# Kernel optimization log

Measured on AMD Instinct MI355X. Metric: run time of the kernel, lower is better.

Reference implementation:

```python
import jax, jax.numpy as jnp
import numpy as np

N = 50000   # nodes
E = 1000000 # edges
D = 64      # input_nf = output_nf = hidden_nf
COORDS_WEIGHT = 1.0


def setup_inputs() -> dict:
    key = jax.random.key(0)
    ks = jax.random.split(key, 16)
    h = jax.random.normal(ks[0], (N, D), dtype=jnp.float32)
    coord = jax.random.normal(ks[1], (N, 3), dtype=jnp.float32)
    edge_index = jax.random.randint(ks[2], (2, E), 0, N, dtype=jnp.int32)
    s = 0.05  # generic init scale
    # edge_mlp: Linear(2D+1 -> D), ReLU, Linear(D -> D), ReLU
    We1 = jax.random.normal(ks[3], (2 * D + 1, D), dtype=jnp.float32) * s
    be1 = jnp.zeros((D,), dtype=jnp.float32)
    We2 = jax.random.normal(ks[4], (D, D), dtype=jnp.float32) * s
    be2 = jnp.zeros((D,), dtype=jnp.float32)
    # node_mlp: Linear(2D -> D), ReLU, Linear(D -> D)
    Wn1 = jax.random.normal(ks[5], (2 * D, D), dtype=jnp.float32) * s
    bn1 = jnp.zeros((D,), dtype=jnp.float32)
    Wn2 = jax.random.normal(ks[6], (D, D), dtype=jnp.float32) * s
    bn2 = jnp.zeros((D,), dtype=jnp.float32)
    # coord_mlp: Linear(D -> D), ReLU, Linear(D -> 1, no bias, xavier gain 0.001)
    Wc1 = jax.random.normal(ks[7], (D, D), dtype=jnp.float32) * s
    bc1 = jnp.zeros((D,), dtype=jnp.float32)
    Wc2 = jax.random.normal(ks[8], (D, 1), dtype=jnp.float32) * 0.001
    return {"h": h, "coord": coord, "edge_index": edge_index,
            "We1": We1, "be1": be1, "We2": We2, "be2": be2,
            "Wn1": Wn1, "bn1": bn1, "Wn2": Wn2, "bn2": bn2,
            "Wc1": Wc1, "bc1": bc1, "Wc2": Wc2}


def reference(h, coord, edge_index, We1, be1, We2, be2, Wn1, bn1, Wn2, bn2, Wc1, bc1, Wc2):
    row, col = edge_index[0], edge_index[1]
    # coord2radial (no PBC offsets; plain pairwise difference)
    coord_diff = coord[row] - coord[col]                    # [E, 3]
    radial = jnp.sum(coord_diff ** 2, axis=1, keepdims=True)  # [E, 1]

    # edge model: MLP on [h_i, h_j, ||x_i - x_j||^2]
    e_in = jnp.concatenate([h[row], h[col], radial], axis=1)  # [E, 2D+1]
    m = jax.nn.relu(e_in @ We1 + be1)
    edge_feat = jax.nn.relu(m @ We2 + be2)                   # [E, D]

    # coord model: per-edge scalar gate, clamp, segment mean
    gate = jax.nn.relu(edge_feat @ Wc1 + bc1) @ Wc2          # [E, 1]
    trans = jnp.clip(coord_diff * gate, -100.0, 100.0)       # [E, 3]
    trans_sum = jax.ops.segment_sum(trans, row, num_segments=N)  # [N, 3]
    cnt = jax.ops.segment_sum(jnp.ones((row.shape[0],), dtype=trans.dtype), row, num_segments=N)
    coord_out = (trans_sum / jnp.maximum(cnt, 1.0)[:, None]) * COORDS_WEIGHT  # [N, 3]

    # node model: scatter-sum aggregate then MLP with residual
    agg = jax.ops.segment_sum(edge_feat, row, num_segments=N)  # [N, D]
    n_in = jnp.concatenate([h, agg], axis=1)                   # [N, 2D]
    h_out = h + (jax.nn.relu(n_in @ Wn1 + bn1) @ Wn2 + bn2)    # residual
    return (h_out, coord_out)
```

## Files before the change

### kernel.cpp

```cpp
#include <hip/hip_runtime.h>

typedef float  f32x4  __attribute__((ext_vector_type(4)));
typedef __bf16 bf16x8 __attribute__((ext_vector_type(8)));
typedef unsigned short u16x8 __attribute__((ext_vector_type(8)));
typedef unsigned int   u32x4 __attribute__((ext_vector_type(4)));

__device__ inline unsigned short f2b(float f) {
    unsigned u = __builtin_bit_cast(unsigned, f);
    u += 0x7fffu + ((u >> 16) & 1u);
    return (unsigned short)(u >> 16);
}

__device__ inline unsigned cvtpk(float a, float b) {
    unsigned r;
    asm("v_cvt_pk_bf16_f32 %0, %1, %2" : "=v"(r) : "v"(a), "v"(b));
    return r;
}

__device__ inline f32x4 mfma16(bf16x8 a, bf16x8 b, f32x4 c) {
    return __builtin_amdgcn_mfma_f32_16x16x32_bf16(a, b, c, 0, 0, 0);
}

__device__ inline bf16x8 cvt8(f32x4 a, f32x4 b) {
    u32x4 w;
    w[0] = cvtpk(a[0], a[1]); w[1] = cvtpk(a[2], a[3]);
    w[2] = cvtpk(b[0], b[1]); w[3] = cvtpk(b[2], b[3]);
    return __builtin_bit_cast(bf16x8, w);
}

__device__ inline bf16x8 ldsA(const unsigned short* base, int frag, int lane) {
    return __builtin_bit_cast(bf16x8,
        *reinterpret_cast<const u16x8*>(base + ((frag * 64 + lane) << 3)));
}

__device__ inline void atom_pk(unsigned short* p, unsigned d) {
    asm volatile("global_atomic_pk_add_bf16 %0, %1, off" :: "v"(p), "v"(d) : "memory");
}

__global__ void k_prep(const float* __restrict__ h, unsigned short* __restrict__ hb,
                       u16x8* __restrict__ aggb8,
                       const int* __restrict__ erow, int* __restrict__ cnt,
                       int n8, int E)
{
    int i = blockIdx.x * 256 + threadIdx.x;
    if (i < n8) {
        const f32x4* p = reinterpret_cast<const f32x4*>(h + (size_t)i * 8);
        bf16x8 v = cvt8(p[0], p[1]);
        reinterpret_cast<u16x8*>(hb)[i] = __builtin_bit_cast(u16x8, v);
        aggb8[i] = (u16x8){0, 0, 0, 0, 0, 0, 0, 0};
    }
    if (i < E) atomicAdd(&cnt[erow[i]], 1);
}

__global__ void k_scanA(const int* __restrict__ cnt, int* __restrict__ bsum, int N)
{
    const int b = blockIdx.x, t = threadIdx.x;
    const int chunk = (N + gridDim.x - 1) / gridDim.x;
    const int lo = b * chunk;
    const int hi = min(lo + chunk, N);
    int s = 0;
    for (int i = lo + t; i < hi; i += 256) s += cnt[i];
#pragma unroll
    for (int d = 1; d < 64; d <<= 1) s += __shfl_xor(s, d, 64);
    __shared__ int ws[4];
    if ((t & 63) == 0) ws[t >> 6] = s;
    __syncthreads();
    if (t == 0) bsum[b] = ws[0] + ws[1] + ws[2] + ws[3];
}

__global__ void k_scanB(const int* __restrict__ cnt, const int* __restrict__ bsum,
                        int* __restrict__ woff, int N)
{
    const int b = blockIdx.x, t = threadIdx.x;
    __shared__ int base_sh;
    __shared__ int ws[4];
    {
        int v = (t < 128 && t < b) ? bsum[t] : 0;
#pragma unroll
        for (int d = 1; d < 64; d <<= 1) v += __shfl_xor(v, d, 64);
        if ((t & 63) == 0) ws[t >> 6] = v;
        __syncthreads();
        if (t == 0) base_sh = ws[0] + ws[1] + ws[2] + ws[3];
        __syncthreads();
    }
    const int base = base_sh;
    const int chunk = (N + gridDim.x - 1) / gridDim.x;
    const int lo = b * chunk;
    const int hi = min(lo + chunk, N);
    const int tchunk = (chunk + 255) / 256;
    const int tlo = lo + t * tchunk;
    const int thi = min(tlo + tchunk, hi);
    int s = 0;
    for (int i = tlo; i < thi; ++i) s += cnt[i];
    const int lane = t & 63, wv = t >> 6;
    int sc = s;
#pragma unroll
    for (int d = 1; d < 64; d <<= 1) { int u = __shfl_up(sc, d, 64); if (lane >= d) sc += u; }
    __shared__ int ws2[4];
    if (lane == 63) ws2[wv] = sc;
    __syncthreads();
    int wadd = 0;
#pragma unroll
    for (int k = 0; k < 4; ++k) wadd += (k < wv) ? ws2[k] : 0;
    int run = base + wadd + (sc - s);
    for (int i = tlo; i < thi; ++i) { woff[i] = run; run += cnt[i]; }
}

__global__ void k_scatter(const int* __restrict__ erow, const int* __restrict__ ecol,
                          int* __restrict__ woff, unsigned* __restrict__ spack,
                          float* __restrict__ cacc, int N, int E)
{
    int i = blockIdx.x * 256 + threadIdx.x;
    if (i < N)
        *reinterpret_cast<f32x4*>(cacc + (size_t)i * 4) = (f32x4){0.f, 0.f, 0.f, 0.f};
    if (i < E) {
        int r = erow[i];
        int pos = atomicAdd(&woff[r], 1);
        spack[pos] = (unsigned)r | ((unsigned)ecol[i] << 16);
    }
}

__global__ __launch_bounds__(512, 2) void egcl_edge_srt(
    const unsigned short* __restrict__ hb,
    const float* __restrict__ coord,
    const unsigned* __restrict__ spack,
    const float* __restrict__ We1, const float* __restrict__ be1,
    const float* __restrict__ We2, const float* __restrict__ be2,
    const float* __restrict__ Wc1, const float* __restrict__ bc1,
    const float* __restrict__ Wc2,
    unsigned short* __restrict__ aggb, float* __restrict__ cacc, int E)
{
    __shared__ __align__(16) unsigned short A1[16 * 512];
    __shared__ __align__(16) unsigned short A2[8 * 512];
    __shared__ __align__(16) unsigned short A3[8 * 512];
    __shared__ __align__(16) float bv[5][64];
    __shared__ __align__(16) unsigned stl[8][34 * 16];

    const int t = threadIdx.x;
    for (int i = t; i < 8192; i += 512) {
        int j = i & 7, lane = (i >> 3) & 63, fi = i >> 9;
        int mt = fi >> 2, ks = fi & 3;
        int in_ch = ks * 32 + ((lane >> 4) << 3) + j;
        int out   = mt * 16 + (lane & 15);
        A1[i] = f2b(We1[in_ch * 64 + out]);
    }
    for (int i = t; i < 4096; i += 512) {
        int j = i & 7, lane = (i >> 3) & 63, fi = i >> 9;
        int mt = fi >> 1, ks = fi & 1;
        int c   = (ks * 2 + (j >> 2)) * 16 + ((lane >> 4) & 3) * 4 + (j & 3);
        int out = mt * 16 + (lane & 15);
        A2[i] = f2b(We2[c * 64 + out]);
        A3[i] = f2b(Wc1[c * 64 + out]);
    }
    if (t < 64) {
        bv[0][t] = be1[t]; bv[1][t] = We1[128 * 64 + t];
        bv[2][t] = be2[t]; bv[3][t] = bc1[t]; bv[4][t] = Wc2[t];
    }
    __syncthreads();

    const int lane = t & 63;
    const int l16 = lane & 15, lq = lane >> 4;
    const int stride = gridDim.x * 8;
    const int wid = (blockIdx.x << 3) + (t >> 6);
    const int ntile = E >> 4;
    const int last = ntile - 1;
    unsigned* st = stl[t >> 6];

    int tile = wid;
    if (tile >= ntile) return;

    int eC = (tile << 4) + l16;
    unsigned pC = spack[eC];
    int rC = (int)(pC & 0xffffu), cC = (int)(pC >> 16);
    u16x8 hr0, hr1, hc0, hc1;
    {
        const u16x8* hr = reinterpret_cast<const u16x8*>(hb + (size_t)rC * 64);
        const u16x8* hc = reinterpret_cast<const u16x8*>(hb + (size_t)cC * 64);
        hr0 = hr[lq]; hr1 = hr[4 + lq]; hc0 = hc[lq]; hc1 = hc[4 + lq];
    }
    float px = 0.f, py = 0.f, pz = 0.f;
    if (lq < 2) {
        int node = (lq == 0) ? rC : cC;
        const float* pp = coord + (size_t)node * 3;
        px = pp[0]; py = pp[1]; pz = pp[2];
    }
    int t1 = tile + stride;
    int tn = (t1 < ntile) ? t1 : last;
    unsigned pN = spack[(tn << 4) + l16];
    int rN = (int)(pN & 0xffffu), cN = (int)(pN >> 16);

    for (; tile < ntile; ) {
        u16x8 nr0, nr1, nc0, nc1;
        {
            const u16x8* hr = reinterpret_cast<const u16x8*>(hb + (size_t)rN * 64);
            const u16x8* hc = reinterpret_cast<const u16x8*>(hb + (size_t)cN * 64);
            nr0 = hr[lq]; nr1 = hr[4 + lq]; nc0 = hc[lq]; nc1 = hc[4 + lq];
        }
        float npx = 0.f, npy = 0.f, npz = 0.f;
        if (lq < 2) {
            int node = (lq == 0) ? rN : cN;
            const float* pp = coord + (size_t)node * 3;
            npx = pp[0]; npy = pp[1]; npz = pp[2];
        }
        int t2 = tile + 2 * stride;
        int t2c = (t2 < ntile) ? t2 : last;
        unsigned pNN = spack[(t2c << 4) + l16];
        int rNN = (int)(pNN & 0xffffu), cNN = (int)(pNN >> 16);

        float prx = __shfl(px, l16, 64), pry = __shfl(py, l16, 64), prz = __shfl(pz, l16, 64);
        float pcx = __shfl(px, 16 + l16, 64), pcy = __shfl(py, 16 + l16, 64), pcz = __shfl(pz, 16 + l16, 64);
        float dx = prx - pcx, dy = pry - pcy, dz = prz - pcz;
        float rad = dx * dx + dy * dy + dz * dz;

        bf16x8 bR[2] = { __builtin_bit_cast(bf16x8, hr0), __builtin_bit_cast(bf16x8, hr1) };
        bf16x8 bC[2] = { __builtin_bit_cast(bf16x8, hc0), __builtin_bit_cast(bf16x8, hc1) };

        f32x4 a1[4];
#pragma unroll
        for (int mt = 0; mt < 4; ++mt)
            a1[mt] = *reinterpret_cast<const f32x4*>(&bv[0][mt * 16 + lq * 4]);
#pragma unroll
        for (int ks = 0; ks < 2; ++ks)
#pragma unroll
            for (int mt = 0; mt < 4; ++mt)
                a1[mt] = mfma16(ldsA(A1, mt * 4 + ks, lane), bR[ks], a1[mt]);
#pragma unroll
        for (int ks = 0; ks < 2; ++ks)
#pragma unroll
            for (int mt = 0; mt < 4; ++mt)
                a1[mt] = mfma16(ldsA(A1, mt * 4 + 2 + ks, lane), bC[ks], a1[mt]);
#pragma unroll
        for (int mt = 0; mt < 4; ++mt) {
            f32x4 wv = *reinterpret_cast<const f32x4*>(&bv[1][mt * 16 + lq * 4]);
#pragma unroll
            for (int rr = 0; rr < 4; ++rr)
                a1[mt][rr] = fmaxf(a1[mt][rr] + rad * wv[rr], 0.f);
        }

        bf16x8 b2[2] = { cvt8(a1[0], a1[1]), cvt8(a1[2], a1[3]) };
        f32x4 a2[4];
#pragma unroll
        for (int mt = 0; mt < 4; ++mt)
            a2[mt] = *reinterpret_cast<const f32x4*>(&bv[2][mt * 16 + lq * 4]);
#pragma unroll
        for (int ks = 0; ks < 2; ++ks)
#pragma unroll
            for (int mt = 0; mt < 4; ++mt)
                a2[mt] = mfma16(ldsA(A2, mt * 2 + ks, lane), b2[ks], a2[mt]);
#pragma unroll
        for (int mt = 0; mt < 4; ++mt)
#pragma unroll
            for (int rr = 0; rr < 4; ++rr)
                a2[mt][rr] = fmaxf(a2[mt][rr], 0.f);

#pragma unroll
        for (int mt = 0; mt < 4; ++mt) {
            int cp0 = mt * 8 + lq * 2;
            int sw  = l16 ^ (cp0 & 12);
            st[(cp0 + 0) * 16 + sw] = cvtpk(a2[mt][0], a2[mt][1]);
            st[(cp0 + 1) * 16 + sw] = cvtpk(a2[mt][2], a2[mt][3]);
        }

        bf16x8 b3[2] = { cvt8(a2[0], a2[1]), cvt8(a2[2], a2[3]) };
        f32x4 a3[4];
#pragma unroll
        for (int mt = 0; mt < 4; ++mt)
            a3[mt] = *reinterpret_cast<const f32x4*>(&bv[3][mt * 16 + lq * 4]);
#pragma unroll
        for (int ks = 0; ks < 2; ++ks)
#pragma unroll
            for (int mt = 0; mt < 4; ++mt)
                a3[mt] = mfma16(ldsA(A3, mt * 2 + ks, lane), b3[ks], a3[mt]);
        float gg = 0.f;
#pragma unroll
        for (int mt = 0; mt < 4; ++mt) {
            f32x4 wv = *reinterpret_cast<const f32x4*>(&bv[4][mt * 16 + lq * 4]);
#pragma unroll
            for (int rr = 0; rr < 4; ++rr)
                gg += fmaxf(a3[mt][rr], 0.f) * wv[rr];
        }
        gg += __shfl_xor(gg, 16, 64);
        gg += __shfl_xor(gg, 32, 64);

        float dsel = (lq == 0) ? dx : (lq == 1) ? dy : dz;
        float val  = fminf(fmaxf(dsel * gg, -100.f), 100.f);

        float vy = __shfl(val, 16 + l16, 64);
        if (lq == 0) st[32 * 16 + l16] = cvtpk(val, vy);
        if (lq == 2) st[33 * 16 + l16] = cvtpk(val, 1.0f);

        u16x8 sv;
#pragma unroll
        for (int j = 0; j < 8; ++j) {
            int ks = lq * 8 + j;
            int rk = __shfl(rC, ks & 15, 64);
            sv[j] = (ks < 16 && rk == rC) ? (unsigned short)0x3F80 : (unsigned short)0;
        }
        bf16x8 self = __builtin_bit_cast(bf16x8, sv);

        f32x4 pg[5];
#pragma unroll
        for (int k = 0; k < 5; ++k) pg[k] = (f32x4){0.f, 0.f, 0.f, 0.f};
        const int elo = (lq & 1) << 3;
#pragma unroll
        for (int tt = 0; tt < 5; ++tt) {
            int cpb = (tt < 4) ? (tt * 8 + (l16 >> 1)) : (32 + ((l16 >> 1) & 1));
            int c   = cpb & 12;
            u32x4 wa = *reinterpret_cast<const u32x4*>(st + cpb * 16 + (elo ^ c));
            u32x4 wb = *reinterpret_cast<const u32x4*>(st + cpb * 16 + ((elo + 4) ^ c));
            u16x8 av;
#pragma unroll
            for (int j = 0; j < 4; ++j) {
                av[j]     = (l16 & 1) ? (unsigned short)(wa[j] >> 16)
                                      : (unsigned short)(wa[j] & 0xffffu);
                av[4 + j] = (l16 & 1) ? (unsigned short)(wb[j] >> 16)
                                      : (unsigned short)(wb[j] & 0xffffu);
            }
            pg[tt] = mfma16(__builtin_bit_cast(bf16x8, av), self, pg[tt]);
        }

#pragma unroll
        for (int mt = 0; mt < 4; ++mt) {
            int cp0 = mt * 8 + lq * 2;
            int sw  = l16 ^ (cp0 & 12);
            st[(cp0 + 0) * 16 + sw] = cvtpk(pg[mt][0], pg[mt][1]);
            st[(cp0 + 1) * 16 + sw] = cvtpk(pg[mt][2], pg[mt][3]);
        }

        int rprev = __shfl(rC, (lane & 48) | ((l16 + 15) & 15), 64);
        bool lead = (l16 == 0) || (rprev != rC);

        if (lead && lq == 0) {
#pragma unroll
            for (int rr = 0; rr < 4; ++rr)
                atomicAdd(&cacc[(size_t)rC * 4 + rr], pg[4][rr]);
        }

        {
            unsigned m = (unsigned)(__ballot(lead) & 0xFFFFull);
            const int cp = lane & 31;
            const int half = lane >> 5;
            while (m) {
                int s0 = __builtin_ctz(m); m &= m - 1;
                int s1 = 16;
                if (m) { s1 = __builtin_ctz(m); m &= m - 1; }
                int s = half ? s1 : s0;
                if (s < 16) {
                    int rw = __shfl(rC, s, 64);
                    unsigned pkd = st[cp * 16 + (s ^ (cp & 12))];
                    atom_pk(aggb + (size_t)rw * 64 + cp * 2, pkd);
                }
            }
        }

        tile = t1; t1 = tile + stride;
        rC = rN; cC = cN; rN = rNN; cN = cNN;
        hr0 = nr0; hr1 = nr1; hc0 = nc0; hc1 = nc1;
        px = npx; py = npy; pz = npz;
    }
}

__global__ __launch_bounds__(512, 4) void egcl_edge_fb(
    const float* __restrict__ h, const float* __restrict__ coord,
    const int* __restrict__ erow, const int* __restrict__ ecol,
    const float* __restrict__ We1, const float* __restrict__ be1,
    const float* __restrict__ We2, const float* __restrict__ be2,
    const float* __restrict__ Wc1, const float* __restrict__ bc1,
    const float* __restrict__ Wc2,
    float* __restrict__ aggf, float* __restrict__ cacc, int E)
{
    __shared__ __align__(16) unsigned short A1[16 * 512];
    __shared__ __align__(16) unsigned short A2[8 * 512];
    __shared__ __align__(16) unsigned short A3[8 * 512];
    __shared__ __align__(16) float bv[5][64];

    const int t = threadIdx.x;
    for (int i = t; i < 8192; i += 512) {
        int j = i & 7, lane = (i >> 3) & 63, fi = i >> 9;
        int mt = fi >> 2, ks = fi & 3;
        int in_ch = ks * 32 + ((lane >> 4) << 3) + j;
        int out   = mt * 16 + (lane & 15);
        A1[i] = f2b(We1[in_ch * 64 + out]);
    }
    for (int i = t; i < 4096; i += 512) {
        int j = i & 7, lane = (i >> 3) & 63, fi = i >> 9;
        int mt = fi >> 1, ks = fi & 1;
        int c   = (ks * 2 + (j >> 2)) * 16 + ((lane >> 4) & 3) * 4 + (j & 3);
        int out = mt * 16 + (lane & 15);
        A2[i] = f2b(We2[c * 64 + out]);
        A3[i] = f2b(Wc1[c * 64 + out]);
    }
    if (t < 64) {
        bv[0][t] = be1[t]; bv[1][t] = We1[128 * 64 + t];
        bv[2][t] = be2[t]; bv[3][t] = bc1[t]; bv[4][t] = Wc2[t];
    }
    __syncthreads();

    const int lane = t & 63;
    const int l16 = lane & 15, lq = lane >> 4;
    const int stride = gridDim.x * 8;
    const int wid = (blockIdx.x << 3) + (t >> 6);
    const int ntile = E >> 4;

    for (int tile = wid; tile < ntile; tile += stride) {
        const int e = (tile << 4) + l16;
        const int r = erow[e], c = ecol[e];
        const float* pr = coord + (size_t)r * 3;
        const float* pc = coord + (size_t)c * 3;
        float dx = pr[0] - pc[0], dy = pr[1] - pc[1], dz = pr[2] - pc[2];
        float rad = dx * dx + dy * dy + dz * dz;
        const f32x4* hr = reinterpret_cast<const f32x4*>(h + (size_t)r * 64);
        const f32x4* hc = reinterpret_cast<const f32x4*>(h + (size_t)c * 64);
        bf16x8 bR[2], bC[2];
#pragma unroll
        for (int ks = 0; ks < 2; ++ks) {
            bR[ks] = cvt8(hr[ks * 8 + lq * 2], hr[ks * 8 + lq * 2 + 1]);
            bC[ks] = cvt8(hc[ks * 8 + lq * 2], hc[ks * 8 + lq * 2 + 1]);
        }
        f32x4 a1[4];
#pragma unroll
        for (int mt = 0; mt < 4; ++mt)
            a1[mt] = *reinterpret_cast<const f32x4*>(&bv[0][mt * 16 + lq * 4]);
#pragma unroll
        for (int ks = 0; ks < 2; ++ks)
#pragma unroll
            for (int mt = 0; mt < 4; ++mt)
                a1[mt] = mfma16(ldsA(A1, mt * 4 + ks, lane), bR[ks], a1[mt]);
#pragma unroll
        for (int ks = 0; ks < 2; ++ks)
#pragma unroll
            for (int mt = 0; mt < 4; ++mt)
                a1[mt] = mfma16(ldsA(A1, mt * 4 + 2 + ks, lane), bC[ks], a1[mt]);
#pragma unroll
        for (int mt = 0; mt < 4; ++mt) {
            f32x4 wv = *reinterpret_cast<const f32x4*>(&bv[1][mt * 16 + lq * 4]);
#pragma unroll
            for (int rr = 0; rr < 4; ++rr)
                a1[mt][rr] = fmaxf(a1[mt][rr] + rad * wv[rr], 0.f);
        }
        bf16x8 b2[2] = { cvt8(a1[0], a1[1]), cvt8(a1[2], a1[3]) };
        f32x4 a2[4];
#pragma unroll
        for (int mt = 0; mt < 4; ++mt)
            a2[mt] = *reinterpret_cast<const f32x4*>(&bv[2][mt * 16 + lq * 4]);
#pragma unroll
        for (int ks = 0; ks < 2; ++ks)
#pragma unroll
            for (int mt = 0; mt < 4; ++mt)
                a2[mt] = mfma16(ldsA(A2, mt * 2 + ks, lane), b2[ks], a2[mt]);
#pragma unroll
        for (int mt = 0; mt < 4; ++mt)
#pragma unroll
            for (int rr = 0; rr < 4; ++rr) {
                a2[mt][rr] = fmaxf(a2[mt][rr], 0.f);
                atomicAdd(&aggf[(size_t)r * 64 + mt * 16 + lq * 4 + rr], a2[mt][rr]);
            }
        bf16x8 b3[2] = { cvt8(a2[0], a2[1]), cvt8(a2[2], a2[3]) };
        f32x4 a3[4];
#pragma unroll
        for (int mt = 0; mt < 4; ++mt)
            a3[mt] = *reinterpret_cast<const f32x4*>(&bv[3][mt * 16 + lq * 4]);
#pragma unroll
        for (int ks = 0; ks < 2; ++ks)
#pragma unroll
            for (int mt = 0; mt < 4; ++mt)
                a3[mt] = mfma16(ldsA(A3, mt * 2 + ks, lane), b3[ks], a3[mt]);
        float gg = 0.f;
#pragma unroll
        for (int mt = 0; mt < 4; ++mt) {
            f32x4 wv = *reinterpret_cast<const f32x4*>(&bv[4][mt * 16 + lq * 4]);
#pragma unroll
            for (int rr = 0; rr < 4; ++rr)
                gg += fmaxf(a3[mt][rr], 0.f) * wv[rr];
        }
        gg += __shfl_xor(gg, 16, 64);
        gg += __shfl_xor(gg, 32, 64);
        float dsel = (lq == 0) ? dx : (lq == 1) ? dy : dz;
        float val  = (lq == 3) ? 1.0f : fminf(fmaxf(dsel * gg, -100.f), 100.f);
        atomicAdd(&cacc[(size_t)r * 4 + lq], val);
    }
}

__device__ inline void stage_wblock(unsigned short* dst, const float* src, int t, int nthr) {
    for (int i = t; i < 4096; i += nthr) {
        int k = i >> 6, n = i & 63;
        int pos = (((n >> 4) * 2 + (k >> 5)) * 64 + ((((k >> 3) & 3) << 4) | (n & 15))) * 8 + (k & 7);
        dst[pos] = f2b(src[i]);
    }
}

__device__ inline bf16x8 ldsB(const unsigned short* base, int nt, int ks, int lane) {
    return __builtin_bit_cast(bf16x8,
        *reinterpret_cast<const u16x8*>(base + (((nt * 2 + ks) * 64 + lane) << 3)));
}

template<bool PK>
__global__ __launch_bounds__(256) void egcl_node(
    const float* __restrict__ h, const unsigned short* __restrict__ hb,
    const float* __restrict__ aggf, const unsigned short* __restrict__ aggb,
    const float* __restrict__ Wn1, const float* __restrict__ bn1,
    const float* __restrict__ Wn2, const float* __restrict__ bn2,
    const float* __restrict__ cacc, float* __restrict__ cout,
    float* __restrict__ hout, int N)
{
    __shared__ __align__(16) unsigned short wlds[3][4096];
    __shared__ __align__(16) unsigned short mlds[4][16 * 72];
    __shared__ float bn1l[64], bn2l[64];

    const int t = threadIdx.x;
    stage_wblock(wlds[0], Wn1, t, 256);
    stage_wblock(wlds[1], Wn1 + 64 * 64, t, 256);
    stage_wblock(wlds[2], Wn2, t, 256);
    if (t < 64) { bn1l[t] = bn1[t]; bn2l[t] = bn2[t]; }
    __syncthreads();

    const int wave = t >> 6, lane = t & 63;
    const int l16 = lane & 15, lq = lane >> 4;
    const int ntile = N >> 4;
    unsigned short* ml = mlds[wave];

    for (int tile = blockIdx.x * 4 + wave; tile < ntile; tile += gridDim.x * 4) {
        const int nb = tile << 4;
        bf16x8 fH[2], fA[2];
        if constexpr (PK) {
            const u16x8* ph = reinterpret_cast<const u16x8*>(hb + (size_t)(nb + l16) * 64);
            const u16x8* pa = reinterpret_cast<const u16x8*>(aggb + (size_t)(nb + l16) * 64);
#pragma unroll
            for (int ks = 0; ks < 2; ++ks) {
                fH[ks] = __builtin_bit_cast(bf16x8, ph[ks * 4 + lq]);
                fA[ks] = __builtin_bit_cast(bf16x8, pa[ks * 4 + lq]);
            }
        } else {
            const f32x4* ph = reinterpret_cast<const f32x4*>(h + (size_t)(nb + l16) * 64);
            const f32x4* pa = reinterpret_cast<const f32x4*>(aggf + (size_t)(nb + l16) * 64);
#pragma unroll
            for (int ks = 0; ks < 2; ++ks) {
                fH[ks] = cvt8(ph[ks * 8 + lq * 2], ph[ks * 8 + lq * 2 + 1]);
                fA[ks] = cvt8(pa[ks * 8 + lq * 2], pa[ks * 8 + lq * 2 + 1]);
            }
        }
        f32x4 acc[4];
#pragma unroll
        for (int nt = 0; nt < 4; ++nt) { float b = bn1l[nt * 16 + l16]; acc[nt] = (f32x4){b, b, b, b}; }
#pragma unroll
        for (int ks = 0; ks < 2; ++ks)
#pragma unroll
            for (int nt = 0; nt < 4; ++nt)
                acc[nt] = mfma16(fH[ks], ldsB(wlds[0], nt, ks, lane), acc[nt]);
#pragma unroll
        for (int ks = 0; ks < 2; ++ks)
#pragma unroll
            for (int nt = 0; nt < 4; ++nt)
                acc[nt] = mfma16(fA[ks], ldsB(wlds[1], nt, ks, lane), acc[nt]);
#pragma unroll
        for (int nt = 0; nt < 4; ++nt)
#pragma unroll
            for (int r = 0; r < 4; ++r)
                ml[(lq * 4 + r) * 72 + nt * 16 + l16] = f2b(fmaxf(acc[nt][r], 0.f));
        bf16x8 fM[2];
#pragma unroll
        for (int ks = 0; ks < 2; ++ks)
            fM[ks] = __builtin_bit_cast(bf16x8,
                *reinterpret_cast<const u16x8*>(ml + l16 * 72 + ks * 32 + lq * 8));
        f32x4 acc2[4];
#pragma unroll
        for (int nt = 0; nt < 4; ++nt) { float b = bn2l[nt * 16 + l16]; acc2[nt] = (f32x4){b, b, b, b}; }
#pragma unroll
        for (int ks = 0; ks < 2; ++ks)
#pragma unroll
            for (int nt = 0; nt < 4; ++nt)
                acc2[nt] = mfma16(fM[ks], ldsB(wlds[2], nt, ks, lane), acc2[nt]);
#pragma unroll
        for (int nt = 0; nt < 4; ++nt)
#pragma unroll
            for (int r = 0; r < 4; ++r) {
                size_t idx = (size_t)(nb + lq * 4 + r) * 64 + nt * 16 + l16;
                hout[idx] = h[idx] + acc2[nt][r];
            }
        if constexpr (PK) {
            if (lq == 0) {
                f32x4 cc = *reinterpret_cast<const f32x4*>(cacc + (size_t)(nb + l16) * 4);
                float inv = 1.f / fmaxf(cc[3], 1.f);
                cout[(size_t)(nb + l16) * 3 + 0] = cc[0] * inv;
                cout[(size_t)(nb + l16) * 3 + 1] = cc[1] * inv;
                cout[(size_t)(nb + l16) * 3 + 2] = cc[2] * inv;
            }
        }
    }
}

__global__ void egcl_coord(const float* __restrict__ cacc, float* __restrict__ cout, int N)
{
    int n = blockIdx.x * 256 + threadIdx.x;
    if (n < N) {
        f32x4 c = *reinterpret_cast<const f32x4*>(cacc + (size_t)n * 4);
        float inv = 1.f / fmaxf(c[3], 1.f);
        cout[n * 3 + 0] = c[0] * inv;
        cout[n * 3 + 1] = c[1] * inv;
        cout[n * 3 + 2] = c[2] * inv;
    }
}

extern "C" void kernel_launch(void* const* d_in, const int* in_sizes, int n_in,
                              void* d_out, int out_size, void* d_ws, size_t ws_size,
                              hipStream_t stream)
{
    const float* h     = (const float*)d_in[0];
    const float* coord = (const float*)d_in[1];
    const int*   eidx  = (const int*)d_in[2];
    const float* We1 = (const float*)d_in[3];  const float* be1 = (const float*)d_in[4];
    const float* We2 = (const float*)d_in[5];  const float* be2 = (const float*)d_in[6];
    const float* Wn1 = (const float*)d_in[7];  const float* bn1 = (const float*)d_in[8];
    const float* Wn2 = (const float*)d_in[9];  const float* bn2 = (const float*)d_in[10];
    const float* Wc1 = (const float*)d_in[11]; const float* bc1 = (const float*)d_in[12];
    const float* Wc2 = (const float*)d_in[13];

    const int N = in_sizes[0] / 64;
    const int E = in_sizes[2] / 2;

    float* hout = (float*)d_out;
    float* cout = hout + (size_t)N * 64;

    const int ntileN = N >> 4;
    const int nblkN  = (ntileN + 3) / 4;

    int*      cnt   = (int*)d_ws;
    float*    cacc  = (float*)d_ws;
    int*      woff  = (int*)((char*)d_ws + (800u << 10));
    int*      bsum  = (int*)((char*)d_ws + (1016u << 10));
    unsigned* spack = (unsigned*)((char*)d_ws + (1u << 20));
    unsigned short* hb   = (unsigned short*)((char*)d_ws + (5u << 20));
    unsigned short* aggb = (unsigned short*)((char*)d_ws + (12u << 20));

    const size_t need_sorted = (12u << 20) + (size_t)N * 128;
    const bool use_sorted = (ws_size >= need_sorted) && N > 0 && (N % 16 == 0)
                            && (N <= 65536) && (E % 16 == 0)
                            && ((size_t)E * 4 <= (4u << 20));

    if (use_sorted) {
        const int n8 = N * 8;
        hipMemsetAsync(cnt, 0, (size_t)N * sizeof(int), stream);
        k_prep<<<(E + 255) / 256, 256, 0, stream>>>(h, hb, (u16x8*)aggb, eidx, cnt, n8, E);
        k_scanA<<<128, 256, 0, stream>>>(cnt, bsum, N);
        k_scanB<<<128, 256, 0, stream>>>(cnt, bsum, woff, N);
        k_scatter<<<(E + 255) / 256, 256, 0, stream>>>(eidx, eidx + E, woff, spack, cacc, N, E);
        egcl_edge_srt<<<2048, 512, 0, stream>>>(hb, coord, spack,
                                                We1, be1, We2, be2, Wc1, bc1, Wc2,
                                                aggb, cacc, E);
        egcl_node<true><<<nblkN, 256, 0, stream>>>(h, hb, nullptr, aggb,
                                                   Wn1, bn1, Wn2, bn2, cacc, cout, hout, N);
    } else {
        float* aggf = hout;
        hipMemsetAsync(cacc, 0, (size_t)N * 4 * sizeof(float), stream);
        hipMemsetAsync(aggf, 0, (size_t)N * 64 * sizeof(float), stream);
        egcl_edge_fb<<<2048, 512, 0, stream>>>(h, coord, eidx, eidx + E,
                                               We1, be1, We2, be2, Wc1, bc1, Wc2,
                                               aggf, cacc, E);
        egcl_node<false><<<nblkN, 256, 0, stream>>>(h, nullptr, aggf, nullptr,
                                                    Wn1, bn1, Wn2, bn2, nullptr, nullptr, hout, N);
        egcl_coord<<<(N + 255) / 256, 256, 0, stream>>>(cacc, cout, N);
    }
}
```

Before: 232.2 us.

## Fuse CSR build kernels into one cooperative kernel with grid syncs

Replaces the memset and the four separate kernels (h conversion plus degree count, two scan passes, scatter into sorted order) with a single cooperative kernel of 512 blocks. The kernel uses grid-stride loops and grid.sync() between phases. The aim is to remove the per-launch and inter-kernel gap overhead on the preprocessing path. In exchange it adds four grid-wide barriers and gives up the occupancy of the larger launch grids for the atomic count and scatter phases.

Result: slower. 469.0 us (+102.0%).

```diff
diff --git a/kernel.cpp b/kernel.cpp
--- a/kernel.cpp
+++ b/kernel.cpp
@@ -1,4 +1,7 @@
 #include <hip/hip_runtime.h>
+#include <hip/hip_cooperative_groups.h>
+
+namespace cg = cooperative_groups;
 
 typedef float  f32x4  __attribute__((ext_vector_type(4)));
 typedef __bf16 bf16x8 __attribute__((ext_vector_type(8)));
@@ -37,83 +40,82 @@
     asm volatile("global_atomic_pk_add_bf16 %0, %1, off" :: "v"(p), "v"(d) : "memory");
 }
 
-__global__ void k_prep(const float* __restrict__ h, unsigned short* __restrict__ hb,
-                       u16x8* __restrict__ aggb8,
-                       const int* __restrict__ erow, int* __restrict__ cnt,
-                       int n8, int E)
+__global__ __launch_bounds__(256, 2) void k_csr(
+    const float* __restrict__ h, unsigned short* __restrict__ hb,
+    u16x8* __restrict__ aggb8, float* __restrict__ cacc,
+    const int* __restrict__ erow, const int* __restrict__ ecol,
+    int* __restrict__ cnt, int* __restrict__ bsum, int* __restrict__ woff,
+    unsigned* __restrict__ spack, int N, int n8, int E)
 {
-    int i = blockIdx.x * 256 + threadIdx.x;
-    if (i < n8) {
+    cg::grid_group grid = cg::this_grid();
+    const int G   = gridDim.x;
+    const int gsz = G * 256;
+    const int gid = blockIdx.x * 256 + threadIdx.x;
+    const int t   = threadIdx.x;
+    const int b   = blockIdx.x;
+    const int lane = t & 63, wv = t >> 6;
+    __shared__ int sh[4];
+
+    for (int i = gid; i < n8; i += gsz) {
         const f32x4* p = reinterpret_cast<const f32x4*>(h + (size_t)i * 8);
         bf16x8 v = cvt8(p[0], p[1]);
         reinterpret_cast<u16x8*>(hb)[i] = __builtin_bit_cast(u16x8, v);
         aggb8[i] = (u16x8){0, 0, 0, 0, 0, 0, 0, 0};
     }
-    if (i < E) atomicAdd(&cnt[erow[i]], 1);
-}
-
-__global__ void k_scanA(const int* __restrict__ cnt, int* __restrict__ bsum, int N)
-{
-    const int b = blockIdx.x, t = threadIdx.x;
-    const int chunk = (N + gridDim.x - 1) / gridDim.x;
-    const int lo = b * chunk;
-    const int hi = min(lo + chunk, N);
-    int s = 0;
-    for (int i = lo + t; i < hi; i += 256) s += cnt[i];
-#pragma unroll
-    for (int d = 1; d < 64; d <<= 1) s += __shfl_xor(s, d, 64);
-    __shared__ int ws[4];
-    if ((t & 63) == 0) ws[t >> 6] = s;
-    __syncthreads();
-    if (t == 0) bsum[b] = ws[0] + ws[1] + ws[2] + ws[3];
-}
-
-__global__ void k_scanB(const int* __restrict__ cnt, const int* __restrict__ bsum,
-                        int* __restrict__ woff, int N)
-{
-    const int b = blockIdx.x, t = threadIdx.x;
-    __shared__ int base_sh;
-    __shared__ int ws[4];
+    for (int i = gid; i < N; i += gsz) cnt[i] = 0;
+    grid.sync();
+
+    for (int i = gid; i < E; i += gsz) atomicAdd(&cnt[erow[i]], 1);
+    grid.sync();
+
+    const int chunk = (N + G - 1) / G;
     {
-        int v = (t < 128 && t < b) ? bsum[t] : 0;
+        const int lo = b * chunk;
+        const int hi = min(lo + chunk, N);
+        int s = 0;
+        for (int i = lo + t; i < hi; i += 256) s += cnt[i];
+#pragma unroll
+        for (int d = 1; d < 64; d <<= 1) s += __shfl_xor(s, d, 64);
+        if (lane == 0) sh[wv] = s;
+        __syncthreads();
+        if (t == 0) bsum[b] = sh[0] + sh[1] + sh[2] + sh[3];
+    }
+    grid.sync();
+
+    {
+        int v = 0;
+        for (int k = t; k < b; k += 256) v += bsum[k];
 #pragma unroll
         for (int d = 1; d < 64; d <<= 1) v += __shfl_xor(v, d, 64);
-        if ((t & 63) == 0) ws[t >> 6] = v;
         __syncthreads();
-        if (t == 0) base_sh = ws[0] + ws[1] + ws[2] + ws[3];
+        if (lane == 0) sh[wv] = v;
         __syncthreads();
-    }
-    const int base = base_sh;
-    const int chunk = (N + gridDim.x - 1) / gridDim.x;
-    const int lo = b * chunk;
-    const int hi = min(lo + chunk, N);
-    const int tchunk = (chunk + 255) / 256;
-    const int tlo = lo + t * tchunk;
-    const int thi = min(tlo + tchunk, hi);
-    int s = 0;
-    for (int i = tlo; i < thi; ++i) s += cnt[i];
-    const int lane = t & 63, wv = t >> 6;
-    int sc = s;
-#pragma unroll
-    for (int d = 1; d < 64; d <<= 1) { int u = __shfl_up(sc, d, 64); if (lane >= d) sc += u; }
-    __shared__ int ws2[4];
-    if (lane == 63) ws2[wv] = sc;
-    __syncthreads();
-    int wadd = 0;
-#pragma unroll
-    for (int k = 0; k < 4; ++k) wadd += (k < wv) ? ws2[k] : 0;
-    int run = base + wadd + (sc - s);
-    for (int i = tlo; i < thi; ++i) { woff[i] = run; run += cnt[i]; }
-}
-
-__global__ void k_scatter(const int* __restrict__ erow, const int* __restrict__ ecol,
-                          int* __restrict__ woff, unsigned* __restrict__ spack,
-                          float* __restrict__ cacc, int N, int E)
-{
-    int i = blockIdx.x * 256 + threadIdx.x;
-    if (i < N)
+        const int base = sh[0] + sh[1] + sh[2] + sh[3];
+
+        const int lo = b * chunk;
+        const int hi = min(lo + chunk, N);
+        const int tchunk = (chunk + 255) / 256;
+        const int tlo = lo + t * tchunk;
+        const int thi = min(tlo + tchunk, hi);
+        int s = 0;
+        for (int i = tlo; i < thi; ++i) s += cnt[i];
+        int sc = s;
+#pragma unroll
+        for (int d = 1; d < 64; d <<= 1) { int u = __shfl_up(sc, d, 64); if (lane >= d) sc += u; }
+        __syncthreads();
+        if (lane == 63) sh[wv] = sc;
+        __syncthreads();
+        int wadd = 0;
+#pragma unroll
+        for (int k = 0; k < 4; ++k) wadd += (k < wv) ? sh[k] : 0;
+        int run = base + wadd + (sc - s);
+        for (int i = tlo; i < thi; ++i) { woff[i] = run; run += cnt[i]; }
+    }
+    grid.sync();
+
+    for (int i = gid; i < N; i += gsz)
         *reinterpret_cast<f32x4*>(cacc + (size_t)i * 4) = (f32x4){0.f, 0.f, 0.f, 0.f};
-    if (i < E) {
+    for (int i = gid; i < E; i += gsz) {
         int r = erow[i];
         int pos = atomicAdd(&woff[r], 1);
         spack[pos] = (unsigned)r | ((unsigned)ecol[i] << 16);
@@ -638,12 +640,16 @@
                             && ((size_t)E * 4 <= (4u << 20));
 
     if (use_sorted) {
-        const int n8 = N * 8;
-        hipMemsetAsync(cnt, 0, (size_t)N * sizeof(int), stream);
-        k_prep<<<(E + 255) / 256, 256, 0, stream>>>(h, hb, (u16x8*)aggb, eidx, cnt, n8, E);
-        k_scanA<<<128, 256, 0, stream>>>(cnt, bsum, N);
-        k_scanB<<<128, 256, 0, stream>>>(cnt, bsum, woff, N);
-        k_scatter<<<(E + 255) / 256, 256, 0, stream>>>(eidx, eidx + E, woff, spack, cacc, N, E);
+        int n8 = N * 8;
+        int N_ = N, E_ = E;
+        const int* erow = eidx;
+        const int* ecol = eidx + E;
+        u16x8* aggb8 = (u16x8*)aggb;
+        void* kargs[] = { (void*)&h, (void*)&hb, (void*)&aggb8, (void*)&cacc,
+                          (void*)&erow, (void*)&ecol, (void*)&cnt, (void*)&bsum,
+                          (void*)&woff, (void*)&spack, (void*)&N_, (void*)&n8, (void*)&E_ };
+        hipLaunchCooperativeKernel((const void*)k_csr, dim3(512), dim3(256),
+                                   kargs, 0, stream);
         egcl_edge_srt<<<2048, 512, 0, stream>>>(hb, coord, spack,
                                                 We1, be1, We2, be2, Wc1, bc1, Wc2,
                                                 aggb, cacc, E);
```
